# Kernel optimization log

Measured on AMD Instinct MI355X. Metric: run time of the kernel, lower is better.

Reference implementation:

```python
import jax, jax.numpy as jnp
import numpy as np

BN_EPS = 1e-5

# Binary_a: sign forward, hard-tanh STE backward (grad zeroed where |x| >= 1)
@jax.custom_vjp
def binary_act(x):
    return jnp.sign(x)

def _ba_fwd(x):
    return jnp.sign(x), x

def _ba_bwd(x, g):
    return (jnp.where((x > -1.0) & (x < 1.0), g, 0.0),)

binary_act.defvjp(_ba_fwd, _ba_bwd)

# Binary_w: sign forward, identity STE backward
@jax.custom_vjp
def binary_w(x):
    return jnp.sign(x)

def _bw_fwd(x):
    return jnp.sign(x), None

def _bw_bwd(_, g):
    return (g,)

binary_w.defvjp(_bw_fwd, _bw_bwd)


def setup_inputs() -> dict:
    key = jax.random.key(0)
    k1, k2, k3 = jax.random.split(key, 3)
    B, Cin, Cout, H, Wd, K = 32, 256, 256, 56, 56, 3
    x = jax.random.normal(k1, (B, Cin, H, Wd), dtype=jnp.float32)
    weight = jax.random.normal(k2, (Cout, Cin, K, K), dtype=jnp.float32) * 0.05
    bias = jax.random.normal(k3, (Cout,), dtype=jnp.float32) * 0.01
    gamma = jnp.ones((Cout,), dtype=jnp.float32)
    beta = jnp.zeros((Cout,), dtype=jnp.float32)
    return {"x": x, "weight": weight, "bias": bias, "gamma": gamma, "beta": beta}


def reference(x, weight, bias, gamma, beta):
    # activation binarization (A=2)
    xb = binary_act(x)
    # weight quantization (W=2): mean-center over in-channel dim, clamp to [-1,1]
    # (done on .data in torch -> values change but no grad through this step)
    wc_val = jnp.clip(weight - jnp.mean(weight, axis=1, keepdims=True), -1.0, 1.0)
    wc = weight + jax.lax.stop_gradient(wc_val - weight)
    # per-output-filter scale alpha = E[|w|] over (in, kh, kw)
    alpha = jnp.mean(jnp.abs(wc), axis=(1, 2, 3), keepdims=True)
    wq = binary_w(wc) * alpha  # [O,I,K,K]
    # conv2d, stride 1, padding 1, groups 1
    y = jax.lax.conv_general_dilated(
        xb, wq, window_strides=(1, 1), padding=((1, 1), (1, 1)),
        dimension_numbers=("NCHW", "OIHW", "NCHW"))
    y = y + bias[None, :, None, None]
    # BatchNorm2d, training-mode forward (biased batch stats)
    mean = jnp.mean(y, axis=(0, 2, 3), keepdims=True)
    var = jnp.mean(jnp.square(y - mean), axis=(0, 2, 3), keepdims=True)
    y = (y - mean) * jax.lax.rsqrt(var + BN_EPS)
    y = y * gamma[None, :, None, None] + beta[None, :, None, None]
    # last_relu=1
    return jax.nn.relu(y)
```

## Files before the change

### kernel.cpp

```cpp
#include <hip/hip_runtime.h>
#include <stdint.h>

typedef unsigned long long u64;
typedef unsigned int u32;
typedef int v4i __attribute__((ext_vector_type(4)));
typedef int v16i __attribute__((ext_vector_type(16)));
typedef short s4v __attribute__((ext_vector_type(4)));
typedef short s8v __attribute__((ext_vector_type(8)));
typedef float f4v __attribute__((ext_vector_type(4)));

#define B_    32
#define CIN   256
#define COUT  256
#define H_    56
#define W_    56
#define HW    3136
#define NPOS  100352
#define HBLK  28
#define NPACKBLK 392


__global__ __launch_bounds__(256) void k_prep(
    const float* __restrict__ x,
    const float* __restrict__ wgt,
    u64* __restrict__ xbits,
    int8_t* __restrict__ Bfrag,
    float* __restrict__ alpha,
    int* __restrict__ ssum,
    unsigned long long* __restrict__ qsum)
{
    const int tid = threadIdx.x;

    if (blockIdx.x < NPACKBLK) {
        const int j = blockIdx.x / 98;
        const int p4 = (blockIdx.x - j * 98) * 256 + tid;
        const int pos0 = p4 * 4;
        const int b = pos0 / HW;
        const int hw = pos0 - b * HW;
        const float* xp = x + (size_t)b * CIN * HW + (size_t)j * 64 * HW + hw;
        u64 b0 = 0, b1 = 0, b2 = 0, b3 = 0;
#pragma unroll 8
        for (int k = 0; k < 64; ++k) {
            const float4 v = *(const float4*)(xp + (size_t)k * HW);
            b0 |= (u64)(v.x > 0.0f) << k;
            b1 |= (u64)(v.y > 0.0f) << k;
            b2 |= (u64)(v.z > 0.0f) << k;
            b3 |= (u64)(v.w > 0.0f) << k;
        }
        xbits[(size_t)pos0 * 4 + j] = b0;
        xbits[(size_t)(pos0 + 1) * 4 + j] = b1;
        xbits[(size_t)(pos0 + 2) * 4 + j] = b2;
        xbits[(size_t)(pos0 + 3) * 4 + j] = b3;
        return;
    }

    const int o = blockIdx.x - NPACKBLK;
    const int i = tid;
    const int wave = i >> 6, lane = i & 63;
    __shared__ float sred[4][12];

    if (i == 0) { ssum[o] = 0; qsum[o] = 0ULL; }

    float w9[9];
#pragma unroll
    for (int t = 0; t < 9; ++t) w9[t] = wgt[(o * 256 + i) * 9 + t];

    float m[9];
#pragma unroll
    for (int t = 0; t < 9; ++t) m[t] = w9[t];
#pragma unroll
    for (int s = 1; s < 64; s <<= 1)
#pragma unroll
        for (int t = 0; t < 9; ++t) m[t] += __shfl_xor(m[t], s, 64);
    if (lane == 0) {
#pragma unroll
        for (int t = 0; t < 9; ++t) sred[wave][t] = m[t];
    }
    __syncthreads();
#pragma unroll
    for (int t = 0; t < 9; ++t)
        m[t] = (sred[0][t] + sred[1][t] + sred[2][t] + sred[3][t]) * (1.0f / 256.0f);

    float wc[9];
    float asum = 0.0f;
#pragma unroll
    for (int t = 0; t < 9; ++t) {
        float v = w9[t] - m[t];
        v = fminf(fmaxf(v, -1.0f), 1.0f);
        wc[t] = v;
        asum += fabsf(v);
    }
#pragma unroll
    for (int s = 1; s < 64; s <<= 1) asum += __shfl_xor(asum, s, 64);
    __syncthreads();
    if (lane == 0) sred[wave][9] = asum;
    __syncthreads();
    if (i == 0)
        alpha[o] = (sred[0][9] + sred[1][9] + sred[2][9] + sred[3][9]) * (1.0f / 2304.0f);

#pragma unroll
    for (int t = 0; t < 9; ++t) {
        const int8_t sv = (wc[t] > 0.0f) ? (int8_t)1 : (int8_t)-1;
        const size_t addr =
            ((size_t)((t * 8 + (i >> 5)) * 8 + (o >> 5)) * 64
             + (size_t)(((i >> 4) & 1) * 32 + (o & 31))) * 16 + (i & 15);
        Bfrag[addr] = sv;
    }
}

#define MFMA_I8(acc, a, b) \
    asm volatile("v_mfma_i32_32x32x32_i8 %0, %1, %2, %0" : "+a"(acc) : "v"(a), "v"(b))

__global__ __launch_bounds__(256, 2) void kc_mfma(
    const u64* __restrict__ xbits,
    const int8_t* __restrict__ Bfrag,
    short* __restrict__ S,
    int* __restrict__ ssum,
    unsigned long long* __restrict__ qsum)
{
    const int blk = blockIdx.x;
    const int b = blk / HBLK;
    const int h0 = (blk - b * HBLK) * 2;
    const int tid = threadIdx.x;

    __shared__ u32 ldsb[4 * 58 * 64];

    for (int it = tid; it < 4 * 58 * 16; it += 256) {
        const int r = it / 928;
        const int rem = it - r * 928;
        const int wp = rem >> 4;
        const int g = rem & 15;
        const int hr = h0 - 1 + r;
        const int w_in = wp - 1;
        const bool inb = (hr >= 0) && (hr < H_) && (w_in >= 0) && (w_in < W_);
        u32 chunk16 = 0;
        if (inb) {
            const u64 word = xbits[((size_t)(b * HW + hr * W_ + w_in)) * 4 + (g >> 2)];
            chunk16 = (u32)(word >> ((g & 3) * 16)) & 0xFFFFu;
        }
        u32 out4[4];
#pragma unroll
        for (int d = 0; d < 4; ++d) {
            const u32 nib = (chunk16 >> (4 * d)) & 0xFu;
            const u32 m1 = (nib * 0x00204081u) & 0x01010101u;
            const u32 inv = m1 ^ 0x01010101u;
            out4[d] = inb ? (0x01010101u ^ (inv * 0xFEu)) : 0u;
        }
        const int gs = (g + wp) & 15;
        u32* dst = &ldsb[((r * 58 + wp) << 6) + gs * 4];
        dst[0] = out4[0]; dst[1] = out4[1]; dst[2] = out4[2]; dst[3] = out4[3];
    }
    __syncthreads();

    const int m0 = tid & 31;
    const int lh = (tid >> 5) & 1;
    const int wv = tid >> 6;
    const int8_t* smem = (const int8_t*)ldsb;
    const int8_t* Bp = Bfrag + (size_t)(tid & 63) * 16;

    auto ldA = [&](int kk, int mt) -> v4i {
        const int tap = kk >> 3, s = kk & 7;
        const int dh = tap / 3;
        const int dw = tap - dh * 3;
        const int r = (mt >> 1) + dh;
        const int wpm = min((mt & 1) * 32 + m0 + dw, 57);
        const int gs = (2 * s + lh + wpm) & 15;
        const int addr = ((r * 58 + wpm) << 8) + (gs << 4);
        return *(const v4i*)(smem + addr);
    };
    auto ldB = [&](int kk, int ntl) -> v4i {
        const size_t off = (size_t)((kk * 8) + wv * 2 + ntl) * 1024;
        return *(const v4i*)(Bp + off);
    };

    v16i acc[4][2] = {};
    v4i A[4][2], Bb[2][2];

#pragma unroll
    for (int mt = 0; mt < 4; ++mt) A[mt][0] = ldA(0, mt);
    Bb[0][0] = ldB(0, 0);
    Bb[1][0] = ldB(0, 1);

#pragma unroll
    for (int kk = 0; kk < 72; ++kk) {
        const int cur = kk & 1, nxt = cur ^ 1;
        if (kk < 71) {
#pragma unroll
            for (int mt = 0; mt < 4; ++mt) A[mt][nxt] = ldA(kk + 1, mt);
            Bb[0][nxt] = ldB(kk + 1, 0);
            Bb[1][nxt] = ldB(kk + 1, 1);
        }
#pragma unroll
        for (int mt = 0; mt < 4; ++mt) {
            MFMA_I8(acc[mt][0], A[mt][cur], Bb[0][cur]);
            MFMA_I8(acc[mt][1], A[mt][cur], Bb[1][cur]);
        }
    }

    asm volatile("s_nop 7\n\ts_nop 7\n\ts_nop 7"
                 : "+a"(acc[0][0]), "+a"(acc[0][1]), "+a"(acc[1][0]), "+a"(acc[1][1]),
                   "+a"(acc[2][0]), "+a"(acc[2][1]), "+a"(acc[3][0]), "+a"(acc[3][1]));

    const int n0 = wv * 64 + m0;
    int s0 = 0, s1 = 0, q0 = 0, q1 = 0;

#pragma unroll
    for (int mt = 0; mt < 4; ++mt) {
        const int h = h0 + (mt >> 1);
        const size_t rowb = (size_t)b * HW + (size_t)h * W_ + ((mt & 1) << 5) + (lh << 2);
        const int nq = (mt & 1) ? 3 : 4;
#pragma unroll
        for (int q = 0; q < nq; ++q) {
            s4v pk0, pk1;
#pragma unroll
            for (int j = 0; j < 4; ++j) {
                const int v0 = acc[mt][0][4 * q + j];
                const int v1 = acc[mt][1][4 * q + j];
                s0 += v0; q0 += v0 * v0; s1 += v1; q1 += v1 * v1;
                pk0[j] = (short)v0;
                pk1[j] = (short)v1;
            }
            *(s4v*)(S + (size_t)n0 * NPOS + rowb + 8 * q) = pk0;
            *(s4v*)(S + (size_t)(n0 + 32) * NPOS + rowb + 8 * q) = pk1;
        }
    }

    s0 += __shfl_xor(s0, 32, 64); q0 += __shfl_xor(q0, 32, 64);
    s1 += __shfl_xor(s1, 32, 64); q1 += __shfl_xor(q1, 32, 64);
    if (lh == 0) {
        atomicAdd(&ssum[n0], s0);
        atomicAdd(&qsum[n0], (unsigned long long)(long long)q0);
        atomicAdd(&ssum[n0 + 32], s1);
        atomicAdd(&qsum[n0 + 32], (unsigned long long)(long long)q1);
    }
}

__global__ __launch_bounds__(256) void kb_apply(
    const short* __restrict__ S,
    const int* __restrict__ ssum,
    const unsigned long long* __restrict__ qsum,
    const float* __restrict__ alpha,
    const float* __restrict__ gamma,
    const float* __restrict__ beta,
    float* __restrict__ out)
{
    const int blk = blockIdx.x;
    const int c = blk >> 5;
    const int b = blk & 31;

    const double N = (double)NPOS;
    const double meanS = (double)ssum[c] / N;
    const double varS = (double)qsum[c] / N - meanS * meanS;
    const double a = (double)alpha[c];
    const double rstd = 1.0 / sqrt(a * a * varS + 1e-5);
    const double g = (double)gamma[c];
    const float scale = (float)(g * a * rstd);
    const float shift = (float)((double)beta[c] - g * a * meanS * rstd);

    const s8v* src = (const s8v*)(S + (size_t)c * NPOS + (size_t)b * HW);
    float* dst = out + ((size_t)(b * COUT + c)) * HW;

    for (int idx = threadIdx.x; idx < HW / 8; idx += 256) {
        const s8v v = src[idx];
        f4v o0, o1;
#pragma unroll
        for (int j = 0; j < 4; ++j)
            o0[j] = fmaxf(fmaf((float)v[j], scale, shift), 0.0f);
#pragma unroll
        for (int j = 0; j < 4; ++j)
            o1[j] = fmaxf(fmaf((float)v[4 + j], scale, shift), 0.0f);
        *(f4v*)(dst + idx * 8) = o0;
        *(f4v*)(dst + idx * 8 + 4) = o1;
    }
}

extern "C" void kernel_launch(void* const* d_in, const int* in_sizes, int n_in,
                              void* d_out, int out_size, void* d_ws, size_t ws_size,
                              hipStream_t stream) {
    const float* x     = (const float*)d_in[0];
    const float* wgt   = (const float*)d_in[1];
    const float* gamma = (const float*)d_in[3];
    const float* beta  = (const float*)d_in[4];
    float* out = (float*)d_out;

    char* ws = (char*)d_ws;
    int8_t* Bfrag = (int8_t*)(ws + 0);
    float* alpha = (float*)(ws + 589824);
    int*   ssum  = (int*)(ws + 590848);
    unsigned long long* qsum = (unsigned long long*)(ws + 591872);
    u64*   xbits = (u64*)(ws + 593920);
    short* Sarr  = (short*)(ws + 3805184);

    k_prep<<<NPACKBLK + 256, 256, 0, stream>>>(x, wgt, xbits, Bfrag, alpha, ssum, qsum);
    kc_mfma<<<B_ * HBLK, 256, 0, stream>>>(xbits, Bfrag, Sarr, ssum, qsum);
    kb_apply<<<COUT * B_, 256, 0, stream>>>(Sarr, ssum, qsum, alpha, gamma, beta, out);
}
```

Before: 286.9 us.

## Restructure bit-packed activation layout, B fragment order, LDS swizzle and staged output stores

Changes xbits to a channel-group-major layout with vectorized 16-byte stores, reorders the weight fragment buffer so each wave reads a contiguous stream, and switches the LDS swizzle from additive to XOR. The MFMA block is bracketed with s_setprio, and the int16 conv results are staged through LDS so global stores become full 16-byte contiguous row segments. The aim is fewer uncoalesced global accesses and fewer LDS bank conflicts, at the cost of extra barriers and LDS traffic in the epilogue.

```diff
diff --git a/kernel.cpp b/kernel.cpp
--- a/kernel.cpp
+++ b/kernel.cpp
@@ -8,6 +8,7 @@
 typedef short s4v __attribute__((ext_vector_type(4)));
 typedef short s8v __attribute__((ext_vector_type(8)));
 typedef float f4v __attribute__((ext_vector_type(4)));
+typedef u64 u64x2 __attribute__((ext_vector_type(2)));
 
 #define B_    32
 #define CIN   256
@@ -47,10 +48,9 @@
             b2 |= (u64)(v.z > 0.0f) << k;
             b3 |= (u64)(v.w > 0.0f) << k;
         }
-        xbits[(size_t)pos0 * 4 + j] = b0;
-        xbits[(size_t)(pos0 + 1) * 4 + j] = b1;
-        xbits[(size_t)(pos0 + 2) * 4 + j] = b2;
-        xbits[(size_t)(pos0 + 3) * 4 + j] = b3;
+        u64* xp4 = xbits + (size_t)j * NPOS + pos0;
+        *(u64x2*)(xp4)     = u64x2{b0, b1};
+        *(u64x2*)(xp4 + 2) = u64x2{b2, b3};
         return;
     }
 
@@ -101,8 +101,9 @@
 #pragma unroll
     for (int t = 0; t < 9; ++t) {
         const int8_t sv = (wc[t] > 0.0f) ? (int8_t)1 : (int8_t)-1;
+        const int kk = t * 8 + (i >> 5);
         const size_t addr =
-            ((size_t)((t * 8 + (i >> 5)) * 8 + (o >> 5)) * 64
+            ((((size_t)(o >> 6) * 72 + kk) * 2 + ((o >> 5) & 1)) * 64
              + (size_t)(((i >> 4) & 1) * 32 + (o & 31))) * 16 + (i & 15);
         Bfrag[addr] = sv;
     }
@@ -135,7 +136,8 @@
         const bool inb = (hr >= 0) && (hr < H_) && (w_in >= 0) && (w_in < W_);
         u32 chunk16 = 0;
         if (inb) {
-            const u64 word = xbits[((size_t)(b * HW + hr * W_ + w_in)) * 4 + (g >> 2)];
+            const u64 word = xbits[(size_t)(g >> 2) * NPOS
+                                   + (size_t)(b * HW + hr * W_ + w_in)];
             chunk16 = (u32)(word >> ((g & 3) * 16)) & 0xFFFFu;
         }
         u32 out4[4];
@@ -146,7 +148,7 @@
             const u32 inv = m1 ^ 0x01010101u;
             out4[d] = inb ? (0x01010101u ^ (inv * 0xFEu)) : 0u;
         }
-        const int gs = (g + wp) & 15;
+        const int gs = (g ^ wp) & 15;
         u32* dst = &ldsb[((r * 58 + wp) << 6) + gs * 4];
         dst[0] = out4[0]; dst[1] = out4[1]; dst[2] = out4[2]; dst[3] = out4[3];
     }
@@ -156,21 +158,19 @@
     const int lh = (tid >> 5) & 1;
     const int wv = tid >> 6;
     const int8_t* smem = (const int8_t*)ldsb;
-    const int8_t* Bp = Bfrag + (size_t)(tid & 63) * 16;
+    const int8_t* Bp = Bfrag + (size_t)wv * 147456 + (size_t)(tid & 63) * 16;
 
     auto ldA = [&](int kk, int mt) -> v4i {
         const int tap = kk >> 3, s = kk & 7;
         const int dh = tap / 3;
         const int dw = tap - dh * 3;
         const int r = (mt >> 1) + dh;
-        const int wpm = min((mt & 1) * 32 + m0 + dw, 57);
-        const int gs = (2 * s + lh + wpm) & 15;
-        const int addr = ((r * 58 + wpm) << 8) + (gs << 4);
-        return *(const v4i*)(smem + addr);
+        const int wpm = (mt & 1) ? min(32 + m0 + dw, 57) : (m0 + dw);
+        const int P = ((r * 58 + wpm) << 8) + ((((wpm & 15) ^ lh)) << 4);
+        return *(const v4i*)(smem + (P ^ (s << 5)));
     };
     auto ldB = [&](int kk, int ntl) -> v4i {
-        const size_t off = (size_t)((kk * 8) + wv * 2 + ntl) * 1024;
-        return *(const v4i*)(Bp + off);
+        return *(const v4i*)(Bp + (size_t)kk * 2048 + ntl * 1024);
     };
 
     v16i acc[4][2] = {};
@@ -190,11 +190,13 @@
             Bb[0][nxt] = ldB(kk + 1, 0);
             Bb[1][nxt] = ldB(kk + 1, 1);
         }
+        __builtin_amdgcn_s_setprio(1);
 #pragma unroll
         for (int mt = 0; mt < 4; ++mt) {
             MFMA_I8(acc[mt][0], A[mt][cur], Bb[0][cur]);
             MFMA_I8(acc[mt][1], A[mt][cur], Bb[1][cur]);
         }
+        __builtin_amdgcn_s_setprio(0);
     }
 
     asm volatile("s_nop 7\n\ts_nop 7\n\ts_nop 7"
@@ -204,10 +206,12 @@
     const int n0 = wv * 64 + m0;
     int s0 = 0, s1 = 0, q0 = 0, q1 = 0;
 
+    __syncthreads();
+    short* eP = (short*)ldsb;
+
 #pragma unroll
     for (int mt = 0; mt < 4; ++mt) {
-        const int h = h0 + (mt >> 1);
-        const size_t rowb = (size_t)b * HW + (size_t)h * W_ + ((mt & 1) << 5) + (lh << 2);
+        const int posb = (mt >> 1) * 56 + ((mt & 1) << 5) + (lh << 2);
         const int nq = (mt & 1) ? 3 : 4;
 #pragma unroll
         for (int q = 0; q < nq; ++q) {
@@ -220,8 +224,25 @@
                 pk0[j] = (short)v0;
                 pk1[j] = (short)v1;
             }
-            *(s4v*)(S + (size_t)n0 * NPOS + rowb + 8 * q) = pk0;
-            *(s4v*)(S + (size_t)(n0 + 32) * NPOS + rowb + 8 * q) = pk1;
+            const int pq = posb + 8 * q;
+            *(s4v*)((char*)eP + n0 * 232 + pq * 2) = pk0;
+            *(s4v*)((char*)eP + (n0 + 32) * 232 + pq * 2) = pk1;
+        }
+    }
+    __syncthreads();
+
+    {
+        const int l = tid & 63;
+        if (l < 56) {
+            const int ch2 = l / 14;
+            const int ii = l - ch2 * 14;
+            const size_t posb2 = (size_t)b * HW + (size_t)h0 * W_;
+#pragma unroll
+            for (int t2 = 0; t2 < 16; ++t2) {
+                const int cg = wv * 64 + t2 * 4 + ch2;
+                const v4i val = *(const v4i*)((const char*)eP + cg * 232 + ii * 16);
+                *(v4i*)(S + (size_t)cg * NPOS + posb2 + ii * 8) = val;
+            }
         }
     }
 
```

Measured after the change: 278.0 us. 3.1% less time.
